# Performance work log

Hardware: AMD Instinct MI355X
Metric: run time of the kernel (lower is better)

## Reference

```python
import jax, jax.numpy as jnp
import numpy as np

IN_DIM, DIM_MSA, PAIR_DIM = 256, 32, 64
B, L = 1, 512


def setup_inputs() -> dict:
    key = jax.random.key(0)
    k0, k1, k2, k3, k4 = jax.random.split(key, 5)
    seq_rep = jax.random.normal(k0, (B, L, IN_DIM), dtype=jnp.float32)
    # torch nn.Linear params: weight [out, in], bias [out]
    s1 = 1.0 / np.sqrt(IN_DIM)
    W1 = jax.random.uniform(k1, (DIM_MSA, IN_DIM), jnp.float32, -s1, s1)
    b1 = jax.random.uniform(k2, (DIM_MSA,), jnp.float32, -s1, s1)
    s2 = 1.0 / np.sqrt(DIM_MSA * DIM_MSA)
    W2 = jax.random.uniform(k3, (PAIR_DIM, DIM_MSA * DIM_MSA), jnp.float32, -s2, s2)
    b2 = jax.random.uniform(k4, (PAIR_DIM,), jnp.float32, -s2, s2)
    return {"seq_rep": seq_rep, "W1": W1, "b1": b1, "W2": W2, "b2": b2}


def reference(seq_rep, W1, b1, W2, b2):
    # proj_down1: [B,L,in_dim] -> [B,L,dim_msa]
    x = seq_rep @ W1.T + b1
    # outer product: 'bid,bjc -> bijcd' then flatten (c d)
    # [B,L(i),L(j),c(dim_msa),d(dim_msa)]
    outer = jnp.einsum('bid,bjc->bijcd', x, x)
    Bb, Li, Lj = outer.shape[:3]
    outer = outer.reshape(Bb, Li, Lj, DIM_MSA * DIM_MSA)  # (c d), c-major
    # proj_down2: -> [B,L,L,pairwise_dim]
    return outer @ W2.T + b2
```

## Files before the change

kernel.cpp:

```cpp
#include <hip/hip_runtime.h>


static constexpr int LL  = 512;
static constexpr int IND = 256;
static constexpr int DM  = 32;
static constexpr int PD  = 64;

typedef _Float16 f16x8 __attribute__((ext_vector_type(8)));
typedef float    f32x16 __attribute__((ext_vector_type(16)));

#define LGKM_BARRIER() do { \
    asm volatile("s_waitcnt lgkmcnt(0)" ::: "memory"); \
    __builtin_amdgcn_s_barrier(); \
  } while (0)

__global__ __launch_bounds__(256) void k_proj1(const float* __restrict__ seq,
                                               const float* __restrict__ W1,
                                               const float* __restrict__ b1,
                                               float* __restrict__ xg,
                                               _Float16* __restrict__ xgh) {
  __shared__ float part[8][DM];
  const int i   = blockIdx.x;
  const int t   = threadIdx.x;
  const int d   = t & 31;
  const int seg = t >> 5;
  const float* srow = seq + (size_t)i * IND + seg * 32;
  const float* wrow = W1  + (size_t)d * IND + seg * 32;
  float acc = 0.f;
#pragma unroll
  for (int k = 0; k < 32; k += 4) {
    const float4 s4 = *(const float4*)(srow + k);
    const float4 w4 = *(const float4*)(wrow + k);
    acc = fmaf(s4.x, w4.x, acc);
    acc = fmaf(s4.y, w4.y, acc);
    acc = fmaf(s4.z, w4.z, acc);
    acc = fmaf(s4.w, w4.w, acc);
  }
  part[seg][d] = acc;
  __syncthreads();
  if (t < DM) {
    float s = b1[t];
#pragma unroll
    for (int g = 0; g < 8; ++g) s += part[g][t];
    xg[i * DM + t]  = s;
    xgh[i * DM + t] = (_Float16)s;
  }
}

__global__ __launch_bounds__(256) void k_y(const float* __restrict__ xg,
                                           const float* __restrict__ W2,
                                           _Float16* __restrict__ Ygh) {
  __shared__ __align__(16) float xs[64][36];
  __shared__ __align__(16) float ws2[64][36];
  const int c     = blockIdx.x & 31;
  const int ibase = (blockIdx.x >> 5) * 64;
  const int t     = threadIdx.x;
#pragma unroll
  for (int k = 0; k < 2; ++k) {
    const int idx = t + k * 256;
    const int il = idx >> 3, d4 = idx & 7;
    const float4 v = *(const float4*)(xg + (size_t)(ibase + il) * DM + d4 * 4);
    *(float4*)&xs[il][d4 * 4] = v;
  }
#pragma unroll
  for (int k = 0; k < 2; ++k) {
    const int idx = t + k * 256;
    const int p = idx >> 3, d4 = idx & 7;
    const float4 v = *(const float4*)(W2 + (size_t)p * (DM * DM) + c * DM + d4 * 4);
    *(float4*)&ws2[p][d4 * 4] = v;
  }
  __syncthreads();
  const int p  = t & 63;
  const int ig = t >> 6;
  float wv[DM];
#pragma unroll
  for (int q = 0; q < 8; ++q) {
    const float4 v = *(const float4*)&ws2[p][q * 4];
    wv[q * 4 + 0] = v.x; wv[q * 4 + 1] = v.y;
    wv[q * 4 + 2] = v.z; wv[q * 4 + 3] = v.w;
  }
#pragma unroll
  for (int il = 0; il < 16; ++il) {
    const int row = ig * 16 + il;
    float a = 0.f;
#pragma unroll
    for (int q = 0; q < 8; ++q) {
      const float4 v = *(const float4*)&xs[row][q * 4];
      a = fmaf(wv[q * 4 + 0], v.x, a);
      a = fmaf(wv[q * 4 + 1], v.y, a);
      a = fmaf(wv[q * 4 + 2], v.z, a);
      a = fmaf(wv[q * 4 + 3], v.w, a);
    }
    Ygh[((size_t)(ibase + row) * DM + c) * PD + p] = (_Float16)a;
  }
}

static constexpr int XPAD = 40;

__global__ __launch_bounds__(128, 3) void k_outer(const _Float16* __restrict__ xgh,
                                                  const _Float16* __restrict__ Ygh,
                                                  const float* __restrict__ b2,
                                                  float* __restrict__ out) {
  __shared__ __align__(16) _Float16 xbs[128 * XPAD];
  __shared__ __align__(16) _Float16 ybs[2 * DM * PD];
  __shared__ __align__(16) float    obuf[32 * PD];
  const int q  = blockIdx.x & 3;
  const int i0 = blockIdx.x >> 2;
  const int t  = threadIdx.x;

  const int lane = t & 63;
  const int w    = t >> 6;
  const int l31  = lane & 31;
  const int lh   = lane >> 5;
  const int pn   = w * 32 + l31;
  const float4 bias4 = *(const float4*)(b2 + (t & 15) * 4);

  {
    const f16x8* src = (const f16x8*)(xgh + (size_t)(q * 128 + t) * DM);
    _Float16* dst = &xbs[t * XPAD];
    *(f16x8*)(dst)      = src[0];
    *(f16x8*)(dst + 8)  = src[1];
    *(f16x8*)(dst + 16) = src[2];
    *(f16x8*)(dst + 24) = src[3];
  }
  {
    const f16x8* ys = (const f16x8*)(Ygh + (size_t)i0 * (DM * PD));
    const f16x8 a = ys[t];
    const f16x8 b = ys[128 + t];
    *(f16x8*)&ybs[t * 8]        = a;
    *(f16x8*)&ybs[1024 + t * 8] = b;
  }
  LGKM_BARRIER();

  const f16x8* ys1 = (const f16x8*)(Ygh + (size_t)(i0 + 256) * (DM * PD));
  const f16x8 n0 = ys1[t];
  const f16x8 n1 = ys1[128 + t];

  auto process = [&](int i, const _Float16* __restrict__ yb) {
    f16x8 b0, b1;
#pragma unroll
    for (int e = 0; e < 8; ++e) {
      b0[e] = yb[(lh * 8 + e) * PD + pn];
      b1[e] = yb[(16 + lh * 8 + e) * PD + pn];
    }
    const size_t orow0 = ((size_t)i * LL + q * 128) * PD;
#pragma unroll
    for (int jt = 0; jt < 4; ++jt) {
      const int ai = (jt * 32 + l31) * XPAD + lh * 8;
      const f16x8 a0 = *(const f16x8*)&xbs[ai];
      const f16x8 a1 = *(const f16x8*)&xbs[ai + 16];
      f32x16 acc = {};
      acc = __builtin_amdgcn_mfma_f32_32x32x16_f16(a0, b0, acc, 0, 0, 0);
      acc = __builtin_amdgcn_mfma_f32_32x32x16_f16(a1, b1, acc, 0, 0, 0);
#pragma unroll
      for (int r = 0; r < 16; ++r) {
        const int row = (r & 3) + 8 * (r >> 2) + 4 * lh;
        obuf[row * PD + pn] = acc[r];
      }
      LGKM_BARRIER();
#pragma unroll
      for (int k = 0; k < 4; ++k) {
        const int idx = t + k * 128;
        float4 v = *(const float4*)&obuf[idx * 4];
        v.x += bias4.x; v.y += bias4.y; v.z += bias4.z; v.w += bias4.w;
        *(float4*)(out + orow0 + (size_t)(jt * 32) * PD + idx * 4) = v;
      }
      LGKM_BARRIER();
    }
  };

  process(i0, ybs);

  *(f16x8*)&ybs[2048 + t * 8]        = n0;
  *(f16x8*)&ybs[2048 + 1024 + t * 8] = n1;
  LGKM_BARRIER();

  process(i0 + 256, ybs + 2048);
}

extern "C" void kernel_launch(void* const* d_in, const int* in_sizes, int n_in,
                              void* d_out, int out_size, void* d_ws, size_t ws_size,
                              hipStream_t stream) {
  const float* seq = (const float*)d_in[0];
  const float* W1  = (const float*)d_in[1];
  const float* b1  = (const float*)d_in[2];
  const float* W2  = (const float*)d_in[3];
  const float* b2  = (const float*)d_in[4];
  float* out = (float*)d_out;

  float* xg     = (float*)d_ws;
  _Float16* xgh = (_Float16*)(xg + LL * DM);
  _Float16* Ygh = (_Float16*)(xg + LL * DM + LL * DM / 2);

  k_proj1<<<LL, 256, 0, stream>>>(seq, W1, b1, xg, xgh);
  k_y<<<256, 256, 0, stream>>>(xg, W2, Ygh);
  k_outer<<<LL * 2, 128, 0, stream>>>(xgh, Ygh, b2, out);
}
```

Baseline: 27.54 us.

## Fuse proj1 into Y kernel and use per-wave output staging without barriers

Merges the first projection and the Y = x·W2 precompute into one kernel, where each block recomputes x for its 16 rows (redundantly across the 32 c-blocks), removing one launch and the fp32 x round trip. In the outer kernel, each wave now stages its own 32x32 output tile in a private LDS buffer, so the two block-wide barriers per tile are dropped. The cost is 32x redundant proj1 compute and W1 reads from global, plus output stores that are less contiguous per instruction (128-byte segments per row instead of full rows).

Result: slower. 77.13 us (+180.0%).

```diff
diff --git a/kernel.cpp b/kernel.cpp
--- a/kernel.cpp
+++ b/kernel.cpp
@@ -14,84 +14,83 @@
     __builtin_amdgcn_s_barrier(); \
   } while (0)
 
-__global__ __launch_bounds__(256) void k_proj1(const float* __restrict__ seq,
-                                               const float* __restrict__ W1,
-                                               const float* __restrict__ b1,
-                                               float* __restrict__ xg,
-                                               _Float16* __restrict__ xgh) {
-  __shared__ float part[8][DM];
-  const int i   = blockIdx.x;
-  const int t   = threadIdx.x;
-  const int d   = t & 31;
-  const int seg = t >> 5;
-  const float* srow = seq + (size_t)i * IND + seg * 32;
-  const float* wrow = W1  + (size_t)d * IND + seg * 32;
-  float acc = 0.f;
+__global__ __launch_bounds__(128) void k_xy(const float* __restrict__ seq,
+                                            const float* __restrict__ W1,
+                                            const float* __restrict__ b1,
+                                            const float* __restrict__ W2,
+                                            _Float16* __restrict__ xgh,
+                                            _Float16* __restrict__ Ygh) {
+  __shared__ __align__(16) float seqs[16][260];
+  __shared__ __align__(16) float ws2[64][36];
+  __shared__ __align__(16) float xs[16][36];
+  const int c     = blockIdx.x & 31;
+  const int ibase = (blockIdx.x >> 5) * 16;
+  const int t     = threadIdx.x;
+
 #pragma unroll
-  for (int k = 0; k < 32; k += 4) {
-    const float4 s4 = *(const float4*)(srow + k);
-    const float4 w4 = *(const float4*)(wrow + k);
-    acc = fmaf(s4.x, w4.x, acc);
-    acc = fmaf(s4.y, w4.y, acc);
-    acc = fmaf(s4.z, w4.z, acc);
-    acc = fmaf(s4.w, w4.w, acc);
-  }
-  part[seg][d] = acc;
-  __syncthreads();
-  if (t < DM) {
-    float s = b1[t];
-#pragma unroll
-    for (int g = 0; g < 8; ++g) s += part[g][t];
-    xg[i * DM + t]  = s;
-    xgh[i * DM + t] = (_Float16)s;
-  }
-}
-
-__global__ __launch_bounds__(256) void k_y(const float* __restrict__ xg,
-                                           const float* __restrict__ W2,
-                                           _Float16* __restrict__ Ygh) {
-  __shared__ __align__(16) float xs[64][36];
-  __shared__ __align__(16) float ws2[64][36];
-  const int c     = blockIdx.x & 31;
-  const int ibase = (blockIdx.x >> 5) * 64;
-  const int t     = threadIdx.x;
-#pragma unroll
-  for (int k = 0; k < 2; ++k) {
-    const int idx = t + k * 256;
-    const int il = idx >> 3, d4 = idx & 7;
-    const float4 v = *(const float4*)(xg + (size_t)(ibase + il) * DM + d4 * 4);
-    *(float4*)&xs[il][d4 * 4] = v;
+  for (int k = 0; k < 8; ++k) {
+    const int idx = t + k * 128;
+    const int row = idx >> 6, j4 = idx & 63;
+    const float4 v = *(const float4*)(seq + (size_t)(ibase + row) * IND + j4 * 4);
+    *(float4*)&seqs[row][j4 * 4] = v;
   }
 #pragma unroll
-  for (int k = 0; k < 2; ++k) {
-    const int idx = t + k * 256;
+  for (int k = 0; k < 4; ++k) {
+    const int idx = t + k * 128;
     const int p = idx >> 3, d4 = idx & 7;
     const float4 v = *(const float4*)(W2 + (size_t)p * (DM * DM) + c * DM + d4 * 4);
     *(float4*)&ws2[p][d4 * 4] = v;
   }
   __syncthreads();
-  const int p  = t & 63;
-  const int ig = t >> 6;
-  float wv[DM];
-#pragma unroll
-  for (int q = 0; q < 8; ++q) {
-    const float4 v = *(const float4*)&ws2[p][q * 4];
-    wv[q * 4 + 0] = v.x; wv[q * 4 + 1] = v.y;
-    wv[q * 4 + 2] = v.z; wv[q * 4 + 3] = v.w;
+
+  {
+    const int row = t >> 3, d0 = (t & 7) * 4;
+    float a0 = b1[d0], a1 = b1[d0 + 1], a2 = b1[d0 + 2], a3 = b1[d0 + 3];
+#pragma unroll 4
+    for (int k4 = 0; k4 < 64; ++k4) {
+      const float4 s = *(const float4*)&seqs[row][k4 * 4];
+      const float4 w0 = *(const float4*)(W1 + (size_t)(d0 + 0) * IND + k4 * 4);
+      const float4 w1 = *(const float4*)(W1 + (size_t)(d0 + 1) * IND + k4 * 4);
+      const float4 w2 = *(const float4*)(W1 + (size_t)(d0 + 2) * IND + k4 * 4);
+      const float4 w3 = *(const float4*)(W1 + (size_t)(d0 + 3) * IND + k4 * 4);
+      a0 = fmaf(s.x, w0.x, fmaf(s.y, w0.y, fmaf(s.z, w0.z, fmaf(s.w, w0.w, a0))));
+      a1 = fmaf(s.x, w1.x, fmaf(s.y, w1.y, fmaf(s.z, w1.z, fmaf(s.w, w1.w, a1))));
+      a2 = fmaf(s.x, w2.x, fmaf(s.y, w2.y, fmaf(s.z, w2.z, fmaf(s.w, w2.w, a2))));
+      a3 = fmaf(s.x, w3.x, fmaf(s.y, w3.y, fmaf(s.z, w3.z, fmaf(s.w, w3.w, a3))));
+    }
+    xs[row][d0 + 0] = a0; xs[row][d0 + 1] = a1;
+    xs[row][d0 + 2] = a2; xs[row][d0 + 3] = a3;
+    if (c == 0) {
+      _Float16* xr = xgh + (size_t)(ibase + row) * DM + d0;
+      xr[0] = (_Float16)a0; xr[1] = (_Float16)a1;
+      xr[2] = (_Float16)a2; xr[3] = (_Float16)a3;
+    }
   }
-#pragma unroll
-  for (int il = 0; il < 16; ++il) {
-    const int row = ig * 16 + il;
-    float a = 0.f;
+  __syncthreads();
+
+  {
+    const int p = t & 63, ih = t >> 6;
+    float wv[DM];
 #pragma unroll
     for (int q = 0; q < 8; ++q) {
-      const float4 v = *(const float4*)&xs[row][q * 4];
-      a = fmaf(wv[q * 4 + 0], v.x, a);
-      a = fmaf(wv[q * 4 + 1], v.y, a);
-      a = fmaf(wv[q * 4 + 2], v.z, a);
-      a = fmaf(wv[q * 4 + 3], v.w, a);
+      const float4 v = *(const float4*)&ws2[p][q * 4];
+      wv[q * 4 + 0] = v.x; wv[q * 4 + 1] = v.y;
+      wv[q * 4 + 2] = v.z; wv[q * 4 + 3] = v.w;
     }
-    Ygh[((size_t)(ibase + row) * DM + c) * PD + p] = (_Float16)a;
+#pragma unroll
+    for (int il = 0; il < 8; ++il) {
+      const int row = ih * 8 + il;
+      float a = 0.f;
+#pragma unroll
+      for (int q = 0; q < 8; ++q) {
+        const float4 v = *(const float4*)&xs[row][q * 4];
+        a = fmaf(wv[q * 4 + 0], v.x, a);
+        a = fmaf(wv[q * 4 + 1], v.y, a);
+        a = fmaf(wv[q * 4 + 2], v.z, a);
+        a = fmaf(wv[q * 4 + 3], v.w, a);
+      }
+      Ygh[((size_t)(ibase + row) * DM + c) * PD + p] = (_Float16)a;
+    }
   }
 }
 
@@ -103,7 +102,7 @@
                                                   float* __restrict__ out) {
   __shared__ __align__(16) _Float16 xbs[128 * XPAD];
   __shared__ __align__(16) _Float16 ybs[2 * DM * PD];
-  __shared__ __align__(16) float    obuf[32 * PD];
+  __shared__ __align__(16) float    obuf[2][32 * 32];
   const int q  = blockIdx.x & 3;
   const int i0 = blockIdx.x >> 2;
   const int t  = threadIdx.x;
@@ -113,7 +112,8 @@
   const int l31  = lane & 31;
   const int lh   = lane >> 5;
   const int pn   = w * 32 + l31;
-  const float4 bias4 = *(const float4*)(b2 + (t & 15) * 4);
+  float* const obufW = &obuf[w][0];
+  const float4 bias4 = *(const float4*)(b2 + w * 32 + (lane & 7) * 4);
 
   {
     const f16x8* src = (const f16x8*)(xgh + (size_t)(q * 128 + t) * DM);
@@ -125,10 +125,8 @@
   }
   {
     const f16x8* ys = (const f16x8*)(Ygh + (size_t)i0 * (DM * PD));
-    const f16x8 a = ys[t];
-    const f16x8 b = ys[128 + t];
-    *(f16x8*)&ybs[t * 8]        = a;
-    *(f16x8*)&ybs[1024 + t * 8] = b;
+    *(f16x8*)&ybs[t * 8]        = ys[t];
+    *(f16x8*)&ybs[1024 + t * 8] = ys[128 + t];
   }
   LGKM_BARRIER();
 
@@ -155,17 +153,16 @@
 #pragma unroll
       for (int r = 0; r < 16; ++r) {
         const int row = (r & 3) + 8 * (r >> 2) + 4 * lh;
-        obuf[row * PD + pn] = acc[r];
+        obufW[row * 32 + l31] = acc[r];
       }
-      LGKM_BARRIER();
 #pragma unroll
       for (int k = 0; k < 4; ++k) {
-        const int idx = t + k * 128;
-        float4 v = *(const float4*)&obuf[idx * 4];
+        const int idx = lane + k * 64;
+        const int row = idx >> 3, pseg = idx & 7;
+        float4 v = *(const float4*)&obufW[idx * 4];
         v.x += bias4.x; v.y += bias4.y; v.z += bias4.z; v.w += bias4.w;
-        *(float4*)(out + orow0 + (size_t)(jt * 32) * PD + idx * 4) = v;
+        *(float4*)(out + orow0 + (size_t)(jt * 32 + row) * PD + w * 32 + pseg * 4) = v;
       }
-      LGKM_BARRIER();
     }
   };
 
@@ -188,11 +185,9 @@
   const float* b2  = (const float*)d_in[4];
   float* out = (float*)d_out;
 
-  float* xg     = (float*)d_ws;
-  _Float16* xgh = (_Float16*)(xg + LL * DM);
-  _Float16* Ygh = (_Float16*)(xg + LL * DM + LL * DM / 2);
+  _Float16* xgh = (_Float16*)d_ws;
+  _Float16* Ygh = xgh + LL * DM;
 
-  k_proj1<<<LL, 256, 0, stream>>>(seq, W1, b1, xg, xgh);
-  k_y<<<256, 256, 0, stream>>>(xg, W2, Ygh);
+  k_xy<<<LL * 2, 128, 0, stream>>>(seq, W1, b1, W2, xgh, Ygh);
   k_outer<<<LL * 2, 128, 0, stream>>>(xgh, Ygh, b2, out);
 }
```
